# Optimization experiments

Measured on AMD Instinct MI355X. Metric: run time of the kernel, lower is better.

Reference implementation:

```python
import jax, jax.numpy as jnp
import numpy as np

N = 65536        # nodes
E = 131072       # directed edges
D = 512          # emb_dim
L = 5            # num_layer
G = 512          # num graphs
EPS = 1e-5       # batchnorm eps
NUM_ATOM_TYPE, NUM_CHIRALITY = 120, 3
NUM_BOND_TYPE, NUM_BOND_DIR = 6, 3


def setup_inputs() -> dict:
    key = jax.random.key(0)
    ks = jax.random.split(key, 12)
    s = 0.02
    return {
        "x": jax.random.randint(ks[0], (N, 2), 0, 3),
        "edge_index": jax.random.randint(ks[1], (2, E), 0, N),
        "edge_attr": jax.random.randint(ks[2], (E, 2), 0, 3),
        "batch": jnp.sort(jax.random.randint(ks[3], (N,), 0, G)),
        "x_emb1": jax.random.normal(ks[4], (NUM_ATOM_TYPE, D), jnp.float32) * s,
        "x_emb2": jax.random.normal(ks[5], (NUM_CHIRALITY, D), jnp.float32) * s,
        "e_emb1": jax.random.normal(ks[6], (L, NUM_BOND_TYPE, D), jnp.float32) * s,
        "e_emb2": jax.random.normal(ks[7], (L, NUM_BOND_DIR, D), jnp.float32) * s,
        "W1": jax.random.normal(ks[8], (L, D, 2 * D), jnp.float32) * s,
        "b1": jnp.zeros((L, 2 * D), jnp.float32),
        "W2": jax.random.normal(ks[9], (L, 2 * D, D), jnp.float32) * s,
        "b2": jnp.zeros((L, D), jnp.float32),
        "gamma": jnp.ones((L, D), jnp.float32),
        "beta": jnp.zeros((L, D), jnp.float32),
    }


def reference(x, edge_index, edge_attr, batch,
              x_emb1, x_emb2, e_emb1, e_emb2,
              W1, b1, W2, b2, gamma, beta):
    n = x.shape[0]
    # atom embedding: type + chirality
    h = x_emb1[x[:, 0]] + x_emb2[x[:, 1]]                     # [N, D]

    # add self loops (appended after real edges, attr = [4, 0])
    loops = jnp.arange(n)
    src = jnp.concatenate([edge_index[0], loops])             # [E+N]
    dst = jnp.concatenate([edge_index[1], loops])
    sl_attr = jnp.concatenate(
        [jnp.full((n, 1), 4, dtype=edge_attr.dtype),
         jnp.zeros((n, 1), dtype=edge_attr.dtype)], axis=1)
    ea = jnp.concatenate([edge_attr, sl_attr], axis=0)        # [E+N, 2]

    for l in range(L):
        # per-edge embedding: bond type + bond direction
        e = e_emb1[l][ea[:, 0]] + e_emb2[l][ea[:, 1]]         # [E+N, D]
        msg = h[src] + e                                      # gather + add
        agg = jax.ops.segment_sum(msg, dst, num_segments=n)   # scatter-add
        # GIN MLP: Linear(D,2D) -> ReLU -> Linear(2D,D)
        hh = jax.nn.relu(agg @ W1[l] + b1[l]) @ W2[l] + b2[l]
        # BatchNorm1d (training-mode batch statistics)
        mean = hh.mean(axis=0)
        var = hh.var(axis=0)
        hh = (hh - mean) * jax.lax.rsqrt(var + EPS) * gamma[l] + beta[l]
        if l < L - 1:
            hh = jax.nn.relu(hh)   # dropout(p=0) is identity
        h = hh

    # JK='last': node rep = h; graph rep = global mean pool over batch ids
    counts = jax.ops.segment_sum(jnp.ones((n,), h.dtype), batch, num_segments=G)
    graph = jax.ops.segment_sum(h, batch, num_segments=G) / jnp.maximum(counts, 1.0)[:, None]
    return graph, h
```

## Files before the change

kernel.cpp:

```cpp
#include <hip/hip_runtime.h>
#include <stdint.h>

#define Nn 65536
#define Ee 131072
#define Dd 512
#define D2 1024
#define Ll 5
#define Gg 512
#define EPSf 1e-5f

typedef _Float16 f16x8 __attribute__((ext_vector_type(8)));
typedef float f32x4 __attribute__((ext_vector_type(4)));
typedef unsigned short u16x8 __attribute__((ext_vector_type(8)));

__device__ __forceinline__ unsigned short f2h(float f) {
    _Float16 h = (_Float16)f;
    union { _Float16 h; unsigned short u; } c; c.h = h;
    return c.u;
}

__device__ __forceinline__ float4 h4f(ushort4 u) {
    union { unsigned short s; _Float16 h; } a, b, c, d;
    a.s = u.x; b.s = u.y; c.s = u.z; d.s = u.w;
    return make_float4((float)a.h, (float)b.h, (float)c.h, (float)d.h);
}

__device__ __forceinline__ void add4(float4& a, float4 b) {
    a.x += b.x; a.y += b.y; a.z += b.z; a.w += b.w;
}

__device__ __forceinline__ void gload_lds16(const void* g, void* l) {
    __builtin_amdgcn_global_load_lds(
        (const __attribute__((address_space(1))) void*)(uintptr_t)g,
        (__attribute__((address_space(3))) void*)(unsigned)(uintptr_t)l,
        16, 0, 0);
}

__global__ void k_transW(const float* __restrict__ src, unsigned short* __restrict__ dst,
                         int K, int Nw) {
    long total = (long)Ll * K * Nw;
    for (long idx = (long)blockIdx.x * blockDim.x + threadIdx.x; idx < total;
         idx += (long)gridDim.x * blockDim.x) {
        long l = idx / ((long)K * Nw);
        long rem = idx - l * (long)K * Nw;
        int k = (int)(rem / Nw), n = (int)(rem % Nw);
        dst[(l * Nw + n) * K + k] = f2h(src[idx]);
    }
}

__global__ void k_embed(const int* __restrict__ x,
                        const float4* __restrict__ xe1, const float4* __restrict__ xe2,
                        float4* __restrict__ h4) {
    const int total = Nn * 128;
    for (int idx = blockIdx.x * blockDim.x + threadIdx.x; idx < total;
         idx += gridDim.x * blockDim.x) {
        int node = idx >> 7, c = idx & 127;
        int t0 = x[2 * node], t1 = x[2 * node + 1];
        float4 v = xe1[t0 * 128 + c];
        float4 w = xe2[t1 * 128 + c];
        v.x += w.x; v.y += w.y; v.z += w.z; v.w += w.w;
        h4[idx] = v;
    }
}

__global__ void k_zeroN(int* __restrict__ p, int n) {
    int i = blockIdx.x * blockDim.x + threadIdx.x;
    if (i < n) p[i] = 0;
}

__global__ void k_hist(const int* __restrict__ edst, int* __restrict__ cnt) {
    int e = blockIdx.x * blockDim.x + threadIdx.x;
    if (e < Ee) atomicAdd(&cnt[edst[e]], 1);
}

__global__ void k_scan(const int* __restrict__ cnt, int* __restrict__ off,
                       int* __restrict__ cursor) {
    __shared__ int part[1024];
    int t = threadIdx.x;
    int base = t * 64;
    int s = 0;
    for (int i = 0; i < 64; ++i) s += cnt[base + i];
    part[t] = s;
    __syncthreads();
    for (int d = 1; d < 1024; d <<= 1) {
        int v = (t >= d) ? part[t - d] : 0;
        __syncthreads();
        part[t] += v;
        __syncthreads();
    }
    int run = part[t] - s;
    for (int i = 0; i < 64; ++i) {
        off[base + i] = run;
        cursor[base + i] = run;
        run += cnt[base + i];
    }
    if (t == 1023) off[Nn] = run;
}

__global__ void k_place(const int* __restrict__ esrc, const int* __restrict__ edst,
                        const int* __restrict__ eattr, int* __restrict__ cursor,
                        int* __restrict__ ckey, int* __restrict__ csrc) {
    int e = blockIdx.x * blockDim.x + threadIdx.x;
    if (e < Ee) {
        int d = edst[e];
        int p = atomicAdd(&cursor[d], 1);
        ckey[p] = e * 32 + (eattr[2 * e] * 3 + eattr[2 * e + 1]);
        csrc[p] = esrc[e];
    }
}

__global__ void k_sort(const int* __restrict__ off, int* __restrict__ ckey,
                       int* __restrict__ csrc) {
    int node = blockIdx.x * blockDim.x + threadIdx.x;
    if (node >= Nn) return;
    int kb = off[node], ke = off[node + 1];
    for (int i = kb + 1; i < ke; ++i) {
        int k = ckey[i], s = csrc[i];
        int j = i - 1;
        while (j >= kb && ckey[j] > k) {
            ckey[j + 1] = ckey[j]; csrc[j + 1] = csrc[j]; --j;
        }
        ckey[j + 1] = k; csrc[j + 1] = s;
    }
}

template <int NORM>
__global__ __launch_bounds__(256) void k_gather(const float* __restrict__ hf32,
                                                const unsigned short* __restrict__ hf16,
                                                const float* __restrict__ ss,
                                                const int* __restrict__ off,
                                                const int* __restrict__ ckey,
                                                const int* __restrict__ csrc,
                                                const float* __restrict__ e1l,
                                                const float* __restrict__ e2l,
                                                unsigned short* __restrict__ aggh) {
    int node = (blockIdx.x << 2) + (threadIdx.x >> 6);
    int lane = threadIdx.x & 63;
    int c0 = lane, c1 = lane + 64;
    float4 sa0, sb0, sa1, sb1;
    if (NORM) {
        const float4* ss4 = (const float4*)ss;
        sa0 = ss4[c0]; sb0 = ss4[128 + c0];
        sa1 = ss4[c1]; sb1 = ss4[128 + c1];
    }
    auto loadrow = [&](size_t rowbase, int c, float4 a, float4 b) -> float4 {
        float4 v;
        if (NORM) {
            v = h4f(*(const ushort4*)(hf16 + rowbase + (size_t)c * 4));
            v.x = fmaxf(fmaf(v.x, a.x, b.x), 0.f);
            v.y = fmaxf(fmaf(v.y, a.y, b.y), 0.f);
            v.z = fmaxf(fmaf(v.z, a.z, b.z), 0.f);
            v.w = fmaxf(fmaf(v.w, a.w, b.w), 0.f);
        } else {
            v = *(const float4*)(hf32 + rowbase + (size_t)c * 4);
        }
        return v;
    };
    const float4* s1 = (const float4*)(e1l + 4 * Dd);
    const float4* s2 = (const float4*)(e2l);
    size_t nb = (size_t)node * Dd;
    float4 A0 = loadrow(nb, c0, sa0, sb0);
    float4 A1 = loadrow(nb, c1, sa1, sb1);
    add4(A0, s1[c0]); add4(A0, s2[c0]);
    add4(A1, s1[c1]); add4(A1, s2[c1]);
    int kb = off[node], ke = off[node + 1];
    for (int k = kb; k < ke; ++k) {
        size_t sb = (size_t)csrc[k] * Dd;
        int at = ckey[k] & 31;
        const float4* p1 = (const float4*)(e1l + (size_t)(at / 3) * Dd);
        const float4* p2 = (const float4*)(e2l + (size_t)(at % 3) * Dd);
        add4(A0, loadrow(sb, c0, sa0, sb0)); add4(A0, p1[c0]); add4(A0, p2[c0]);
        add4(A1, loadrow(sb, c1, sa1, sb1)); add4(A1, p1[c1]); add4(A1, p2[c1]);
    }
    unsigned short* dst = aggh + (size_t)node * Dd;
    ushort4 o0, o1;
    o0.x = f2h(A0.x); o0.y = f2h(A0.y); o0.z = f2h(A0.z); o0.w = f2h(A0.w);
    o1.x = f2h(A1.x); o1.y = f2h(A1.y); o1.z = f2h(A1.z); o1.w = f2h(A1.w);
    *(ushort4*)(dst + c0 * 4) = o0;
    *(ushort4*)(dst + c1 * 4) = o1;
}

__device__ __forceinline__ void stage_q(const unsigned short* __restrict__ g, int ldk,
                                        long row0, int col0, char* region, int tid) {
    int wbase = (tid >> 6) << 10;
#pragma unroll
    for (int r = 0; r < 2; ++r) {
        int gi = tid + r * 512;
        int row = gi >> 2;
        int k16 = (gi & 3) ^ ((row >> 1) & 3);
        gload_lds16(g + (row0 + row) * (long)ldk + col0 + k16 * 8,
                    region + r * 8192 + wbase);
    }
}

__device__ __forceinline__ f16x8 rd_frag(const char* region, int row, int l4) {
    int slot = l4 ^ ((row >> 1) & 3);
    return *(const f16x8*)(region + row * 64 + (slot << 4));
}

template <int EPI>
__global__ __launch_bounds__(512, 2) void gemm8(const unsigned short* __restrict__ A,
                                                const unsigned short* __restrict__ BT,
                                                const float* __restrict__ bias,
                                                unsigned short* __restrict__ Cb,
                                                float* __restrict__ pS,
                                                int M, int N, int K) {
    __shared__ __align__(16) char lds[131072];
    const int tid = threadIdx.x;
    const int lane = tid & 63;
    const int w = tid >> 6;
    const int wm = w >> 2, wn = w & 3;
    const int l15 = lane & 15, l4 = lane >> 4;

    const int nwg = gridDim.x;
    const int cpx = nwg >> 3;
    const int bid = blockIdx.x;
    const int wg = (bid & 7) * cpx + (bid >> 3);
    const int ntn = N >> 8;
    const long bm = (long)(wg / ntn) * 256;
    const long bn = (long)(wg % ntn) * 256;

    char* Ar = lds;
    char* Br = lds + 65536;
    const int NT = K >> 6;

    f32x4 acc[8][4];
#pragma unroll
    for (int i = 0; i < 8; ++i)
#pragma unroll
        for (int j = 0; j < 4; ++j) acc[i][j] = (f32x4){0.f, 0.f, 0.f, 0.f};

    stage_q(A, K, bm, 0, Ar, tid);
    stage_q(BT, K, bn, 0, Br, tid);
    stage_q(A, K, bm, 32, Ar + 16384, tid);
    stage_q(BT, K, bn, 32, Br + 16384, tid);
    asm volatile("s_waitcnt vmcnt(4)" ::: "memory");
    __builtin_amdgcn_s_barrier();
    asm volatile("" ::: "memory");

    for (int t = 0; t < NT; ++t) {
        const int par = (t & 1) << 15;
        const int npar = ((t + 1) & 1) << 15;
        const bool pre = (t + 1 < NT);
#pragma unroll
        for (int kh = 0; kh < 2; ++kh) {
            const char* Ac = Ar + par + kh * 16384;
            const char* Bc = Br + par + kh * 16384;
            f16x8 af[8], bv[4];
#pragma unroll
            for (int fn = 0; fn < 4; ++fn)
                bv[fn] = rd_frag(Bc, wn * 64 + fn * 16 + l15, l4);
#pragma unroll
            for (int fm = 0; fm < 8; ++fm)
                af[fm] = rd_frag(Ac, wm * 128 + fm * 16 + l15, l4);
            if (pre) {
                stage_q(BT, K, bn, (t + 1) * 64 + kh * 32, Br + npar + kh * 16384, tid);
                stage_q(A, K, bm, (t + 1) * 64 + kh * 32, Ar + npar + kh * 16384, tid);
            }
#pragma unroll
            for (int fm = 0; fm < 8; ++fm)
#pragma unroll
                for (int fn = 0; fn < 4; ++fn)
                    acc[fm][fn] = __builtin_amdgcn_mfma_f32_16x16x32_f16(af[fm], bv[fn], acc[fm][fn], 0, 0, 0);
            if (pre) {
                asm volatile("s_waitcnt vmcnt(4)" ::: "memory");
            } else {
                asm volatile("s_waitcnt vmcnt(0)" ::: "memory");
            }
            __builtin_amdgcn_s_barrier();
            asm volatile("" ::: "memory");
        }
    }

    unsigned short* cl = (unsigned short*)lds;
    float cs[4] = {0.f, 0.f, 0.f, 0.f}, cq[4] = {0.f, 0.f, 0.f, 0.f};
#pragma unroll
    for (int hh = 0; hh < 2; ++hh) {
        __syncthreads();
        if (wm == hh) {
#pragma unroll
            for (int fn = 0; fn < 4; ++fn) {
                int col = wn * 64 + fn * 16 + l15;
                float bval = bias[bn + col];
#pragma unroll
                for (int fm = 0; fm < 8; ++fm) {
                    int r0 = fm * 16 + l4 * 4;
#pragma unroll
                    for (int r = 0; r < 4; ++r) {
                        float v = acc[fm][fn][r] + bval;
                        if (EPI == 0) v = fmaxf(v, 0.f);
                        else { cs[fn] += v; cq[fn] += v * v; }
                        cl[(r0 + r) * 264 + col] = f2h(v);
                    }
                }
            }
        }
        __syncthreads();
#pragma unroll
        for (int i = 0; i < 8; ++i) {
            int g = tid + i * 512;
            int r = g >> 5, cg = (g & 31) << 3;
            u16x8 val = *(const u16x8*)&cl[r * 264 + cg];
            *(u16x8*)&Cb[(bm + hh * 128 + r) * N + bn + cg] = val;
        }
    }
    if (EPI == 1) {
#pragma unroll
        for (int fn = 0; fn < 4; ++fn) {
            float s = cs[fn], q = cq[fn];
            s += __shfl_xor(s, 16); s += __shfl_xor(s, 32);
            q += __shfl_xor(q, 16); q += __shfl_xor(q, 32);
            if (l4 == 0) {
                int col = (int)bn + wn * 64 + fn * 16 + l15;
                int rowgrp = ((int)(bm >> 8)) * 2 + wm;
                pS[rowgrp * 512 + col] = s;
                pS[262144 + rowgrp * 512 + col] = q;
            }
        }
    }
}

__global__ void k_bnred(const float* __restrict__ pS, const float* __restrict__ gamma,
                        const float* __restrict__ beta, float* __restrict__ ss) {
    int col = blockIdx.x * 256 + threadIdx.x;
    float s = 0.f, q = 0.f;
    for (int rg = 0; rg < 512; ++rg) {
        s += pS[rg * 512 + col];
        q += pS[262144 + rg * 512 + col];
    }
    float mean = s * (1.f / (float)Nn);
    float var = q * (1.f / (float)Nn) - mean * mean;
    float a = gamma[col] * rsqrtf(var + EPSf);
    ss[col] = a;
    ss[512 + col] = beta[col] - mean * a;
}

__global__ void k_norm(const unsigned short* __restrict__ hhf, const float* __restrict__ ss,
                       float4* __restrict__ h4) {
    const int total = Nn * 128;
    const float4* ss4 = (const float4*)ss;
    for (int idx = blockIdx.x * blockDim.x + threadIdx.x; idx < total;
         idx += gridDim.x * blockDim.x) {
        int c = idx & 127;
        float4 v = h4f(*(const ushort4*)(hhf + (size_t)idx * 4));
        float4 a = ss4[c], b = ss4[128 + c];
        v.x = fmaf(v.x, a.x, b.x); v.y = fmaf(v.y, a.y, b.y);
        v.z = fmaf(v.z, a.z, b.z); v.w = fmaf(v.w, a.w, b.w);
        h4[idx] = v;
    }
}

__global__ void k_pool(const unsigned short* __restrict__ hhf, const float* __restrict__ ss,
                       const int* __restrict__ batch, float* __restrict__ graph) {
    int g = blockIdx.x, t = threadIdx.x;
    int lo = 0, hi = Nn;
    while (lo < hi) { int m = (lo + hi) >> 1; if (batch[m] < g) lo = m + 1; else hi = m; }
    int s = lo;
    lo = s; hi = Nn;
    while (lo < hi) { int m = (lo + hi) >> 1; if (batch[m] <= g) lo = m + 1; else hi = m; }
    int e = lo;
    float a0 = ss[t], a1 = ss[t + 256];
    float b0 = ss[512 + t], b1 = ss[512 + t + 256];
    union { unsigned short s; _Float16 h; } u0, u1;
    float s0 = 0.f, s1 = 0.f;
    for (int r = s; r < e; ++r) {
        const unsigned short* row = hhf + (size_t)r * Dd;
        u0.s = row[t]; u1.s = row[t + 256];
        s0 += fmaf((float)u0.h, a0, b0);
        s1 += fmaf((float)u1.h, a1, b1);
    }
    int cnt = e - s; if (cnt < 1) cnt = 1;
    float inv = 1.f / (float)cnt;
    graph[(long)g * Dd + t] = s0 * inv;
    graph[(long)g * Dd + t + 256] = s1 * inv;
}

extern "C" void kernel_launch(void* const* d_in, const int* in_sizes, int n_in,
                              void* d_out, int out_size, void* d_ws, size_t ws_size,
                              hipStream_t stream) {
    (void)in_sizes; (void)n_in; (void)out_size; (void)ws_size;
    const int* x      = (const int*)d_in[0];
    const int* ei     = (const int*)d_in[1];
    const int* ea     = (const int*)d_in[2];
    const int* batch  = (const int*)d_in[3];
    const float* xe1  = (const float*)d_in[4];
    const float* xe2  = (const float*)d_in[5];
    const float* ee1  = (const float*)d_in[6];
    const float* ee2  = (const float*)d_in[7];
    const float* W1   = (const float*)d_in[8];
    const float* b1   = (const float*)d_in[9];
    const float* W2   = (const float*)d_in[10];
    const float* b2   = (const float*)d_in[11];
    const float* gamma = (const float*)d_in[12];
    const float* beta  = (const float*)d_in[13];

    float* graph = (float*)d_out;
    float* h = graph + (size_t)Gg * Dd;

    char* w = (char*)d_ws;
    int* csr_off = (int*)w;                     w += (Nn + 1) * 4;
    int* cursor = (int*)w;                      w += Nn * 4;
    int* cnt = (int*)w;                         w += Nn * 4;
    int* ckey = (int*)w;                        w += Ee * 4;
    int* csrc = (int*)w;                        w += Ee * 4;
    float* ss = (float*)w;                      w += 4096;
    float* pS = (float*)w;                      w += 2 * 512 * 512 * 4;
    unsigned short* aggh = (unsigned short*)w;  w += (size_t)Nn * Dd * 2;
    unsigned short* hhf = (unsigned short*)w;   w += (size_t)Nn * Dd * 2;
    unsigned short* w1t = (unsigned short*)w;   w += (size_t)Ll * D2 * Dd * 2;
    unsigned short* w2t = (unsigned short*)w;   w += (size_t)Ll * Dd * D2 * 2;

    k_transW<<<2048, 256, 0, stream>>>(W1, w1t, Dd, D2);
    k_transW<<<2048, 256, 0, stream>>>(W2, w2t, D2, Dd);

    k_embed<<<2048, 256, 0, stream>>>(x, (const float4*)xe1, (const float4*)xe2, (float4*)h);

    k_zeroN<<<64, 1024, 0, stream>>>(cnt, Nn);
    k_hist<<<Ee / 256, 256, 0, stream>>>(ei + Ee, cnt);
    k_scan<<<1, 1024, 0, stream>>>(cnt, csr_off, cursor);
    k_place<<<Ee / 256, 256, 0, stream>>>(ei, ei + Ee, ea, cursor, ckey, csrc);
    k_sort<<<Nn / 256, 256, 0, stream>>>(csr_off, ckey, csrc);

    for (int l = 0; l < Ll; ++l) {
        const float* e1l = ee1 + (size_t)l * 6 * Dd;
        const float* e2l = ee2 + (size_t)l * 3 * Dd;
        if (l == 0)
            k_gather<0><<<Nn / 4, 256, 0, stream>>>(h, nullptr, nullptr, csr_off, ckey, csrc,
                                                    e1l, e2l, aggh);
        else
            k_gather<1><<<Nn / 4, 256, 0, stream>>>(nullptr, hhf, ss, csr_off, ckey, csrc,
                                                    e1l, e2l, aggh);
        gemm8<0><<<(Nn / 256) * (D2 / 256), 512, 0, stream>>>(
            aggh, w1t + (size_t)l * D2 * Dd, b1 + (size_t)l * D2,
            (unsigned short*)h, nullptr, Nn, D2, Dd);
        gemm8<1><<<(Nn / 256) * (Dd / 256), 512, 0, stream>>>(
            (const unsigned short*)h, w2t + (size_t)l * Dd * D2, b2 + (size_t)l * Dd,
            hhf, pS, Nn, Dd, D2);
        k_bnred<<<2, 256, 0, stream>>>(pS, gamma + (size_t)l * Dd, beta + (size_t)l * Dd, ss);
    }

    k_norm<<<2048, 256, 0, stream>>>(hhf, ss, (float4*)h);
    k_pool<<<Gg, 256, 0, stream>>>(hhf, ss, batch, graph);
}
```

Before: 1.622 ms.

## Shrink GEMM tile to 128x128 with 256 threads and triple-buffered K pipeline

Replaces the 256x256-tile, 512-thread GEMM with a 128x128-tile, 256-thread kernel. It uses a three-slot LDS ring of 32-wide K chunks, prefetching two steps ahead, and a single-pass epilogue. The BN partial-sum buffer doubles to 1024 row groups, and the reduction kernel loops over all of them. Smaller tiles cut LDS use (48KB vs 128KB) so more blocks fit per CU, at the cost of lower per-tile data reuse and more global loads.

```diff
diff --git a/kernel.cpp b/kernel.cpp
--- a/kernel.cpp
+++ b/kernel.cpp
@@ -185,11 +185,11 @@
     int wbase = (tid >> 6) << 10;
 #pragma unroll
     for (int r = 0; r < 2; ++r) {
-        int gi = tid + r * 512;
+        int gi = tid + r * 256;
         int row = gi >> 2;
         int k16 = (gi & 3) ^ ((row >> 1) & 3);
         gload_lds16(g + (row0 + row) * (long)ldk + col0 + k16 * 8,
-                    region + r * 8192 + wbase);
+                    region + r * 4096 + wbase);
     }
 }
 
@@ -199,110 +199,100 @@
 }
 
 template <int EPI>
-__global__ __launch_bounds__(512, 2) void gemm8(const unsigned short* __restrict__ A,
+__global__ __launch_bounds__(256, 2) void gemm4(const unsigned short* __restrict__ A,
                                                 const unsigned short* __restrict__ BT,
                                                 const float* __restrict__ bias,
                                                 unsigned short* __restrict__ Cb,
                                                 float* __restrict__ pS,
                                                 int M, int N, int K) {
-    __shared__ __align__(16) char lds[131072];
+    __shared__ __align__(16) char lds[49152];
     const int tid = threadIdx.x;
     const int lane = tid & 63;
     const int w = tid >> 6;
-    const int wm = w >> 2, wn = w & 3;
+    const int wm = w >> 1, wn = w & 1;
     const int l15 = lane & 15, l4 = lane >> 4;
 
     const int nwg = gridDim.x;
     const int cpx = nwg >> 3;
     const int bid = blockIdx.x;
     const int wg = (bid & 7) * cpx + (bid >> 3);
-    const int ntn = N >> 8;
-    const long bm = (long)(wg / ntn) * 256;
-    const long bn = (long)(wg % ntn) * 256;
-
-    char* Ar = lds;
-    char* Br = lds + 65536;
-    const int NT = K >> 6;
-
-    f32x4 acc[8][4];
-#pragma unroll
-    for (int i = 0; i < 8; ++i)
+    const int ntn = N >> 7;
+    const long bm = (long)(wg / ntn) * 128;
+    const long bn = (long)(wg % ntn) * 128;
+
+    const int NT = K >> 5;
+
+    f32x4 acc[4][4];
+#pragma unroll
+    for (int i = 0; i < 4; ++i)
 #pragma unroll
         for (int j = 0; j < 4; ++j) acc[i][j] = (f32x4){0.f, 0.f, 0.f, 0.f};
 
-    stage_q(A, K, bm, 0, Ar, tid);
-    stage_q(BT, K, bn, 0, Br, tid);
-    stage_q(A, K, bm, 32, Ar + 16384, tid);
-    stage_q(BT, K, bn, 32, Br + 16384, tid);
+    stage_q(A, K, bm, 0, lds, tid);
+    stage_q(BT, K, bn, 0, lds + 8192, tid);
+    stage_q(A, K, bm, 32, lds + 16384, tid);
+    stage_q(BT, K, bn, 32, lds + 16384 + 8192, tid);
     asm volatile("s_waitcnt vmcnt(4)" ::: "memory");
     __builtin_amdgcn_s_barrier();
     asm volatile("" ::: "memory");
 
+    int cur = 0, nx2 = 2;
     for (int t = 0; t < NT; ++t) {
-        const int par = (t & 1) << 15;
-        const int npar = ((t + 1) & 1) << 15;
-        const bool pre = (t + 1 < NT);
-#pragma unroll
-        for (int kh = 0; kh < 2; ++kh) {
-            const char* Ac = Ar + par + kh * 16384;
-            const char* Bc = Br + par + kh * 16384;
-            f16x8 af[8], bv[4];
+        const char* Ac = lds + cur * 16384;
+        const char* Bc = Ac + 8192;
+        f16x8 af[4], bv[4];
+#pragma unroll
+        for (int fn = 0; fn < 4; ++fn)
+            bv[fn] = rd_frag(Bc, wn * 64 + fn * 16 + l15, l4);
+#pragma unroll
+        for (int fm = 0; fm < 4; ++fm)
+            af[fm] = rd_frag(Ac, wm * 64 + fm * 16 + l15, l4);
+        if (t + 2 < NT) {
+            char* dst = lds + nx2 * 16384;
+            stage_q(A, K, bm, (t + 2) * 32, dst, tid);
+            stage_q(BT, K, bn, (t + 2) * 32, dst + 8192, tid);
+        }
+#pragma unroll
+        for (int fm = 0; fm < 4; ++fm)
 #pragma unroll
             for (int fn = 0; fn < 4; ++fn)
-                bv[fn] = rd_frag(Bc, wn * 64 + fn * 16 + l15, l4);
-#pragma unroll
-            for (int fm = 0; fm < 8; ++fm)
-                af[fm] = rd_frag(Ac, wm * 128 + fm * 16 + l15, l4);
-            if (pre) {
-                stage_q(BT, K, bn, (t + 1) * 64 + kh * 32, Br + npar + kh * 16384, tid);
-                stage_q(A, K, bm, (t + 1) * 64 + kh * 32, Ar + npar + kh * 16384, tid);
-            }
-#pragma unroll
-            for (int fm = 0; fm < 8; ++fm)
-#pragma unroll
-                for (int fn = 0; fn < 4; ++fn)
-                    acc[fm][fn] = __builtin_amdgcn_mfma_f32_16x16x32_f16(af[fm], bv[fn], acc[fm][fn], 0, 0, 0);
-            if (pre) {
-                asm volatile("s_waitcnt vmcnt(4)" ::: "memory");
-            } else {
-                asm volatile("s_waitcnt vmcnt(0)" ::: "memory");
-            }
-            __builtin_amdgcn_s_barrier();
-            asm volatile("" ::: "memory");
-        }
+                acc[fm][fn] = __builtin_amdgcn_mfma_f32_16x16x32_f16(af[fm], bv[fn], acc[fm][fn], 0, 0, 0);
+        if (t + 2 < NT) {
+            asm volatile("s_waitcnt vmcnt(4)" ::: "memory");
+        } else {
+            asm volatile("s_waitcnt vmcnt(0)" ::: "memory");
+        }
+        __builtin_amdgcn_s_barrier();
+        asm volatile("" ::: "memory");
+        cur = (cur == 2) ? 0 : cur + 1;
+        nx2 = (nx2 == 2) ? 0 : nx2 + 1;
     }
 
     unsigned short* cl = (unsigned short*)lds;
     float cs[4] = {0.f, 0.f, 0.f, 0.f}, cq[4] = {0.f, 0.f, 0.f, 0.f};
 #pragma unroll
-    for (int hh = 0; hh < 2; ++hh) {
-        __syncthreads();
-        if (wm == hh) {
-#pragma unroll
-            for (int fn = 0; fn < 4; ++fn) {
-                int col = wn * 64 + fn * 16 + l15;
-                float bval = bias[bn + col];
-#pragma unroll
-                for (int fm = 0; fm < 8; ++fm) {
-                    int r0 = fm * 16 + l4 * 4;
-#pragma unroll
-                    for (int r = 0; r < 4; ++r) {
-                        float v = acc[fm][fn][r] + bval;
-                        if (EPI == 0) v = fmaxf(v, 0.f);
-                        else { cs[fn] += v; cq[fn] += v * v; }
-                        cl[(r0 + r) * 264 + col] = f2h(v);
-                    }
-                }
+    for (int fn = 0; fn < 4; ++fn) {
+        int col = wn * 64 + fn * 16 + l15;
+        float bval = bias[bn + col];
+#pragma unroll
+        for (int fm = 0; fm < 4; ++fm) {
+            int r0 = wm * 64 + fm * 16 + l4 * 4;
+#pragma unroll
+            for (int r = 0; r < 4; ++r) {
+                float v = acc[fm][fn][r] + bval;
+                if (EPI == 0) v = fmaxf(v, 0.f);
+                else { cs[fn] += v; cq[fn] += v * v; }
+                cl[(r0 + r) * 136 + col] = f2h(v);
             }
         }
-        __syncthreads();
-#pragma unroll
-        for (int i = 0; i < 8; ++i) {
-            int g = tid + i * 512;
-            int r = g >> 5, cg = (g & 31) << 3;
-            u16x8 val = *(const u16x8*)&cl[r * 264 + cg];
-            *(u16x8*)&Cb[(bm + hh * 128 + r) * N + bn + cg] = val;
-        }
+    }
+    __syncthreads();
+#pragma unroll
+    for (int i = 0; i < 8; ++i) {
+        int g = tid + i * 256;
+        int r = g >> 4, cg = (g & 15) << 3;
+        u16x8 val = *(const u16x8*)&cl[r * 136 + cg];
+        *(u16x8*)&Cb[(bm + r) * N + bn + cg] = val;
     }
     if (EPI == 1) {
 #pragma unroll
@@ -312,9 +302,9 @@
             q += __shfl_xor(q, 16); q += __shfl_xor(q, 32);
             if (l4 == 0) {
                 int col = (int)bn + wn * 64 + fn * 16 + l15;
-                int rowgrp = ((int)(bm >> 8)) * 2 + wm;
+                int rowgrp = (int)(bm >> 6) + wm;
                 pS[rowgrp * 512 + col] = s;
-                pS[262144 + rowgrp * 512 + col] = q;
+                pS[524288 + rowgrp * 512 + col] = q;
             }
         }
     }
@@ -324,9 +314,9 @@
                         const float* __restrict__ beta, float* __restrict__ ss) {
     int col = blockIdx.x * 256 + threadIdx.x;
     float s = 0.f, q = 0.f;
-    for (int rg = 0; rg < 512; ++rg) {
+    for (int rg = 0; rg < 1024; ++rg) {
         s += pS[rg * 512 + col];
-        q += pS[262144 + rg * 512 + col];
+        q += pS[524288 + rg * 512 + col];
     }
     float mean = s * (1.f / (float)Nn);
     float var = q * (1.f / (float)Nn) - mean * mean;
@@ -404,7 +394,7 @@
     int* ckey = (int*)w;                        w += Ee * 4;
     int* csrc = (int*)w;                        w += Ee * 4;
     float* ss = (float*)w;                      w += 4096;
-    float* pS = (float*)w;                      w += 2 * 512 * 512 * 4;
+    float* pS = (float*)w;                      w += 2 * 1024 * 512 * 4;
     unsigned short* aggh = (unsigned short*)w;  w += (size_t)Nn * Dd * 2;
     unsigned short* hhf = (unsigned short*)w;   w += (size_t)Nn * Dd * 2;
     unsigned short* w1t = (unsigned short*)w;   w += (size_t)Ll * D2 * Dd * 2;
@@ -430,10 +420,10 @@
         else
             k_gather<1><<<Nn / 4, 256, 0, stream>>>(nullptr, hhf, ss, csr_off, ckey, csrc,
                                                     e1l, e2l, aggh);
-        gemm8<0><<<(Nn / 256) * (D2 / 256), 512, 0, stream>>>(
+        gemm4<0><<<(Nn / 128) * (D2 / 128), 256, 0, stream>>>(
             aggh, w1t + (size_t)l * D2 * Dd, b1 + (size_t)l * D2,
             (unsigned short*)h, nullptr, Nn, D2, Dd);
-        gemm8<1><<<(Nn / 256) * (Dd / 256), 512, 0, stream>>>(
+        gemm4<1><<<(Nn / 128) * (Dd / 128), 256, 0, stream>>>(
             (const unsigned short*)h, w2t + (size_t)l * Dd * D2, b2 + (size_t)l * Dd,
             hhf, pS, Nn, Dd, D2);
         k_bnred<<<2, 256, 0, stream>>>(pS, gamma + (size_t)l * Dd, beta + (size_t)l * Dd, ss);
```

After: 1.846 ms. 13.8% more time.

## Precombine edge embeddings, widen gather to 8 halves, split BN reduction

Applied to the files above, without the earlier changes.

Builds a per-layer table of the 18 combined bond-type plus bond-direction embeddings, so each edge does one table row load instead of two. The gather kernel now has each lane handle 8 contiguous fp16 values with 16-byte loads. The initial node embedding is written as fp16, which halves that read in layer 0. The batchnorm stat reduction, previously 2 blocks each looping over 512 row groups, becomes a 64-block partial pass followed by a 1-block final pass to add parallelism. Rounding layer-0 inputs to fp16 adds a small precision loss.

```diff
diff --git a/kernel.cpp b/kernel.cpp
--- a/kernel.cpp
+++ b/kernel.cpp
@@ -19,14 +19,9 @@
     return c.u;
 }
 
-__device__ __forceinline__ float4 h4f(ushort4 u) {
-    union { unsigned short s; _Float16 h; } a, b, c, d;
-    a.s = u.x; b.s = u.y; c.s = u.z; d.s = u.w;
-    return make_float4((float)a.h, (float)b.h, (float)c.h, (float)d.h);
-}
-
-__device__ __forceinline__ void add4(float4& a, float4 b) {
-    a.x += b.x; a.y += b.y; a.z += b.z; a.w += b.w;
+__device__ __forceinline__ float h2f(unsigned short s) {
+    union { unsigned short s; _Float16 h; } c; c.s = s;
+    return (float)c.h;
 }
 
 __device__ __forceinline__ void gload_lds16(const void* g, void* l) {
@@ -48,18 +43,36 @@
     }
 }
 
+__global__ void k_etab(const float* __restrict__ ee1, const float* __restrict__ ee2,
+                       float* __restrict__ E) {
+    int idx = blockIdx.x * blockDim.x + threadIdx.x;
+    const int total = Ll * 18 * Dd;
+    if (idx < total) {
+        int l = idx / (18 * Dd);
+        int rem = idx - l * 18 * Dd;
+        int j = rem / Dd, c = rem - j * Dd;
+        int a0 = j / 3, a1 = j - a0 * 3;
+        E[idx] = ee1[((size_t)l * 6 + a0) * Dd + c] + ee2[((size_t)l * 3 + a1) * Dd + c];
+    }
+}
+
 __global__ void k_embed(const int* __restrict__ x,
-                        const float4* __restrict__ xe1, const float4* __restrict__ xe2,
-                        float4* __restrict__ h4) {
-    const int total = Nn * 128;
+                        const float* __restrict__ xe1, const float* __restrict__ xe2,
+                        unsigned short* __restrict__ hhf) {
+    const int total = Nn * 64;
     for (int idx = blockIdx.x * blockDim.x + threadIdx.x; idx < total;
          idx += gridDim.x * blockDim.x) {
-        int node = idx >> 7, c = idx & 127;
+        int node = idx >> 6, c8 = (idx & 63) * 8;
         int t0 = x[2 * node], t1 = x[2 * node + 1];
-        float4 v = xe1[t0 * 128 + c];
-        float4 w = xe2[t1 * 128 + c];
-        v.x += w.x; v.y += w.y; v.z += w.z; v.w += w.w;
-        h4[idx] = v;
+        const float4* p1 = (const float4*)(xe1 + (size_t)t0 * Dd + c8);
+        const float4* p2 = (const float4*)(xe2 + (size_t)t1 * Dd + c8);
+        float4 a0 = p1[0], a1 = p1[1], b0 = p2[0], b1 = p2[1];
+        u16x8 o;
+        o[0] = f2h(a0.x + b0.x); o[1] = f2h(a0.y + b0.y);
+        o[2] = f2h(a0.z + b0.z); o[3] = f2h(a0.w + b0.w);
+        o[4] = f2h(a1.x + b1.x); o[5] = f2h(a1.y + b1.y);
+        o[6] = f2h(a1.z + b1.z); o[7] = f2h(a1.w + b1.w);
+        *(u16x8*)(hhf + (size_t)node * Dd + c8) = o;
     }
 }
 
@@ -125,59 +138,62 @@
 }
 
 template <int NORM>
-__global__ __launch_bounds__(256) void k_gather(const float* __restrict__ hf32,
-                                                const unsigned short* __restrict__ hf16,
+__global__ __launch_bounds__(256) void k_gather(const unsigned short* __restrict__ hf16,
                                                 const float* __restrict__ ss,
                                                 const int* __restrict__ off,
                                                 const int* __restrict__ ckey,
                                                 const int* __restrict__ csrc,
-                                                const float* __restrict__ e1l,
-                                                const float* __restrict__ e2l,
+                                                const float* __restrict__ El,
                                                 unsigned short* __restrict__ aggh) {
     int node = (blockIdx.x << 2) + (threadIdx.x >> 6);
     int lane = threadIdx.x & 63;
-    int c0 = lane, c1 = lane + 64;
-    float4 sa0, sb0, sa1, sb1;
+    int c8 = lane * 8;
+    float sa[8], sb[8];
     if (NORM) {
-        const float4* ss4 = (const float4*)ss;
-        sa0 = ss4[c0]; sb0 = ss4[128 + c0];
-        sa1 = ss4[c1]; sb1 = ss4[128 + c1];
-    }
-    auto loadrow = [&](size_t rowbase, int c, float4 a, float4 b) -> float4 {
-        float4 v;
-        if (NORM) {
-            v = h4f(*(const ushort4*)(hf16 + rowbase + (size_t)c * 4));
-            v.x = fmaxf(fmaf(v.x, a.x, b.x), 0.f);
-            v.y = fmaxf(fmaf(v.y, a.y, b.y), 0.f);
-            v.z = fmaxf(fmaf(v.z, a.z, b.z), 0.f);
-            v.w = fmaxf(fmaf(v.w, a.w, b.w), 0.f);
-        } else {
-            v = *(const float4*)(hf32 + rowbase + (size_t)c * 4);
-        }
-        return v;
-    };
-    const float4* s1 = (const float4*)(e1l + 4 * Dd);
-    const float4* s2 = (const float4*)(e2l);
-    size_t nb = (size_t)node * Dd;
-    float4 A0 = loadrow(nb, c0, sa0, sb0);
-    float4 A1 = loadrow(nb, c1, sa1, sb1);
-    add4(A0, s1[c0]); add4(A0, s2[c0]);
-    add4(A1, s1[c1]); add4(A1, s2[c1]);
+        float4 a0 = *(const float4*)(ss + c8), a1 = *(const float4*)(ss + c8 + 4);
+        float4 b0 = *(const float4*)(ss + 512 + c8), b1 = *(const float4*)(ss + 512 + c8 + 4);
+        sa[0] = a0.x; sa[1] = a0.y; sa[2] = a0.z; sa[3] = a0.w;
+        sa[4] = a1.x; sa[5] = a1.y; sa[6] = a1.z; sa[7] = a1.w;
+        sb[0] = b0.x; sb[1] = b0.y; sb[2] = b0.z; sb[3] = b0.w;
+        sb[4] = b1.x; sb[5] = b1.y; sb[6] = b1.z; sb[7] = b1.w;
+    }
+    float acc[8];
+    {
+        u16x8 v = *(const u16x8*)(hf16 + (size_t)node * Dd + c8);
+        float4 e0 = *(const float4*)(El + 12 * Dd + c8);
+        float4 e1 = *(const float4*)(El + 12 * Dd + c8 + 4);
+        float ev[8];
+        ev[0] = e0.x; ev[1] = e0.y; ev[2] = e0.z; ev[3] = e0.w;
+        ev[4] = e1.x; ev[5] = e1.y; ev[6] = e1.z; ev[7] = e1.w;
+#pragma unroll
+        for (int i = 0; i < 8; ++i) {
+            float hv = h2f(v[i]);
+            if (NORM) hv = fmaxf(fmaf(hv, sa[i], sb[i]), 0.f);
+            acc[i] = hv + ev[i];
+        }
+    }
     int kb = off[node], ke = off[node + 1];
     for (int k = kb; k < ke; ++k) {
-        size_t sb = (size_t)csrc[k] * Dd;
+        int src = csrc[k];
         int at = ckey[k] & 31;
-        const float4* p1 = (const float4*)(e1l + (size_t)(at / 3) * Dd);
-        const float4* p2 = (const float4*)(e2l + (size_t)(at % 3) * Dd);
-        add4(A0, loadrow(sb, c0, sa0, sb0)); add4(A0, p1[c0]); add4(A0, p2[c0]);
-        add4(A1, loadrow(sb, c1, sa1, sb1)); add4(A1, p1[c1]); add4(A1, p2[c1]);
-    }
-    unsigned short* dst = aggh + (size_t)node * Dd;
-    ushort4 o0, o1;
-    o0.x = f2h(A0.x); o0.y = f2h(A0.y); o0.z = f2h(A0.z); o0.w = f2h(A0.w);
-    o1.x = f2h(A1.x); o1.y = f2h(A1.y); o1.z = f2h(A1.z); o1.w = f2h(A1.w);
-    *(ushort4*)(dst + c0 * 4) = o0;
-    *(ushort4*)(dst + c1 * 4) = o1;
+        u16x8 v = *(const u16x8*)(hf16 + (size_t)src * Dd + c8);
+        const float* Er = El + (size_t)at * Dd + c8;
+        float4 e0 = *(const float4*)(Er);
+        float4 e1 = *(const float4*)(Er + 4);
+        float ev[8];
+        ev[0] = e0.x; ev[1] = e0.y; ev[2] = e0.z; ev[3] = e0.w;
+        ev[4] = e1.x; ev[5] = e1.y; ev[6] = e1.z; ev[7] = e1.w;
+#pragma unroll
+        for (int i = 0; i < 8; ++i) {
+            float hv = h2f(v[i]);
+            if (NORM) hv = fmaxf(fmaf(hv, sa[i], sb[i]), 0.f);
+            acc[i] += hv + ev[i];
+        }
+    }
+    u16x8 o;
+#pragma unroll
+    for (int i = 0; i < 8; ++i) o[i] = f2h(acc[i]);
+    *(u16x8*)(aggh + (size_t)node * Dd + c8) = o;
 }
 
 __device__ __forceinline__ void stage_q(const unsigned short* __restrict__ g, int ldk,
@@ -320,19 +336,37 @@
     }
 }
 
-__global__ void k_bnred(const float* __restrict__ pS, const float* __restrict__ gamma,
-                        const float* __restrict__ beta, float* __restrict__ ss) {
-    int col = blockIdx.x * 256 + threadIdx.x;
+__global__ void k_bnA(const float* __restrict__ pS, float* __restrict__ pT) {
+    int b = blockIdx.x;
+    int t = threadIdx.x;
+    float s0 = 0.f, s1 = 0.f, q0 = 0.f, q1 = 0.f;
+#pragma unroll
+    for (int i = 0; i < 8; ++i) {
+        int rg = b * 8 + i;
+        s0 += pS[rg * 512 + t];
+        s1 += pS[rg * 512 + t + 256];
+        q0 += pS[262144 + rg * 512 + t];
+        q1 += pS[262144 + rg * 512 + t + 256];
+    }
+    pT[b * 512 + t] = s0;
+    pT[b * 512 + t + 256] = s1;
+    pT[32768 + b * 512 + t] = q0;
+    pT[32768 + b * 512 + t + 256] = q1;
+}
+
+__global__ void k_bnB(const float* __restrict__ pT, const float* __restrict__ gamma,
+                      const float* __restrict__ beta, float* __restrict__ ss) {
+    int c = threadIdx.x;
     float s = 0.f, q = 0.f;
-    for (int rg = 0; rg < 512; ++rg) {
-        s += pS[rg * 512 + col];
-        q += pS[262144 + rg * 512 + col];
+    for (int b = 0; b < 64; ++b) {
+        s += pT[b * 512 + c];
+        q += pT[32768 + b * 512 + c];
     }
     float mean = s * (1.f / (float)Nn);
     float var = q * (1.f / (float)Nn) - mean * mean;
-    float a = gamma[col] * rsqrtf(var + EPSf);
-    ss[col] = a;
-    ss[512 + col] = beta[col] - mean * a;
+    float a = gamma[c] * rsqrtf(var + EPSf);
+    ss[c] = a;
+    ss[512 + c] = beta[c] - mean * a;
 }
 
 __global__ void k_norm(const unsigned short* __restrict__ hhf, const float* __restrict__ ss,
@@ -342,7 +376,8 @@
     for (int idx = blockIdx.x * blockDim.x + threadIdx.x; idx < total;
          idx += gridDim.x * blockDim.x) {
         int c = idx & 127;
-        float4 v = h4f(*(const ushort4*)(hhf + (size_t)idx * 4));
+        ushort4 u = *(const ushort4*)(hhf + (size_t)idx * 4);
+        float4 v = make_float4(h2f(u.x), h2f(u.y), h2f(u.z), h2f(u.w));
         float4 a = ss4[c], b = ss4[128 + c];
         v.x = fmaf(v.x, a.x, b.x); v.y = fmaf(v.y, a.y, b.y);
         v.z = fmaf(v.z, a.z, b.z); v.w = fmaf(v.w, a.w, b.w);
@@ -361,13 +396,11 @@
     int e = lo;
     float a0 = ss[t], a1 = ss[t + 256];
     float b0 = ss[512 + t], b1 = ss[512 + t + 256];
-    union { unsigned short s; _Float16 h; } u0, u1;
     float s0 = 0.f, s1 = 0.f;
     for (int r = s; r < e; ++r) {
         const unsigned short* row = hhf + (size_t)r * Dd;
-        u0.s = row[t]; u1.s = row[t + 256];
-        s0 += fmaf((float)u0.h, a0, b0);
-        s1 += fmaf((float)u1.h, a1, b1);
+        s0 += fmaf(h2f(row[t]), a0, b0);
+        s1 += fmaf(h2f(row[t + 256]), a1, b1);
     }
     int cnt = e - s; if (cnt < 1) cnt = 1;
     float inv = 1.f / (float)cnt;
@@ -405,6 +438,8 @@
     int* csrc = (int*)w;                        w += Ee * 4;
     float* ss = (float*)w;                      w += 4096;
     float* pS = (float*)w;                      w += 2 * 512 * 512 * 4;
+    float* pT = (float*)w;                      w += 2 * 64 * 512 * 4;
+    float* Etab = (float*)w;                    w += (size_t)Ll * 18 * Dd * 4;
     unsigned short* aggh = (unsigned short*)w;  w += (size_t)Nn * Dd * 2;
     unsigned short* hhf = (unsigned short*)w;   w += (size_t)Nn * Dd * 2;
     unsigned short* w1t = (unsigned short*)w;   w += (size_t)Ll * D2 * Dd * 2;
@@ -412,8 +447,8 @@
 
     k_transW<<<2048, 256, 0, stream>>>(W1, w1t, Dd, D2);
     k_transW<<<2048, 256, 0, stream>>>(W2, w2t, D2, Dd);
-
-    k_embed<<<2048, 256, 0, stream>>>(x, (const float4*)xe1, (const float4*)xe2, (float4*)h);
+    k_etab<<<(Ll * 18 * Dd + 255) / 256, 256, 0, stream>>>(ee1, ee2, Etab);
+    k_embed<<<2048, 256, 0, stream>>>(x, xe1, xe2, hhf);
 
     k_zeroN<<<64, 1024, 0, stream>>>(cnt, Nn);
     k_hist<<<Ee / 256, 256, 0, stream>>>(ei + Ee, cnt);
@@ -422,21 +457,21 @@
     k_sort<<<Nn / 256, 256, 0, stream>>>(csr_off, ckey, csrc);
 
     for (int l = 0; l < Ll; ++l) {
-        const float* e1l = ee1 + (size_t)l * 6 * Dd;
-        const float* e2l = ee2 + (size_t)l * 3 * Dd;
+        const float* El = Etab + (size_t)l * 18 * Dd;
         if (l == 0)
-            k_gather<0><<<Nn / 4, 256, 0, stream>>>(h, nullptr, nullptr, csr_off, ckey, csrc,
-                                                    e1l, e2l, aggh);
+            k_gather<0><<<Nn / 4, 256, 0, stream>>>(hhf, nullptr, csr_off, ckey, csrc,
+                                                    El, aggh);
         else
-            k_gather<1><<<Nn / 4, 256, 0, stream>>>(nullptr, hhf, ss, csr_off, ckey, csrc,
-                                                    e1l, e2l, aggh);
+            k_gather<1><<<Nn / 4, 256, 0, stream>>>(hhf, ss, csr_off, ckey, csrc,
+                                                    El, aggh);
         gemm8<0><<<(Nn / 256) * (D2 / 256), 512, 0, stream>>>(
             aggh, w1t + (size_t)l * D2 * Dd, b1 + (size_t)l * D2,
             (unsigned short*)h, nullptr, Nn, D2, Dd);
         gemm8<1><<<(Nn / 256) * (Dd / 256), 512, 0, stream>>>(
             (const unsigned short*)h, w2t + (size_t)l * Dd * D2, b2 + (size_t)l * Dd,
             hhf, pS, Nn, Dd, D2);
-        k_bnred<<<2, 256, 0, stream>>>(pS, gamma + (size_t)l * Dd, beta + (size_t)l * Dd, ss);
+        k_bnA<<<64, 256, 0, stream>>>(pS, pT);
+        k_bnB<<<1, 512, 0, stream>>>(pT, gamma + (size_t)l * Dd, beta + (size_t)l * Dd, ss);
     }
 
     k_norm<<<2048, 256, 0, stream>>>(hhf, ss, (float4*)h);
```

New measurement: 1.433 ms. -11.6%, faster.
